# Kernel tuning notes

Hardware: AMD Instinct MI355X
Metric: run time of the kernel (lower is better)

Reference implementation:

```python
import jax, jax.numpy as jnp
import numpy as np

L, B, S, D, H, FF = 6, 32, 512, 512, 8, 2048
DK = D // H
EPS = 1e-5
GELU_C = 0.7978845608028654  # sqrt(2/pi)
INV_SQRT_DK = 1.0 / float(np.sqrt(DK))


def gelu(x):
    return 0.5 * x * (1.0 + jnp.tanh(GELU_C * (x + 0.044715 * x ** 3)))


def layernorm(x, gamma, beta):
    m = jnp.mean(x, axis=-1, keepdims=True)
    v = jnp.mean(jnp.square(x - m), axis=-1, keepdims=True)
    return gamma * (x - m) / jnp.sqrt(v + EPS) + beta


def attention(x, WQ, WK, WV, WO):
    # NOTE: the original splits columns as (d_key, n_heads) on input,
    # and merges as (n_heads * d_key) on output -- replicated faithfully.
    q = (x @ WQ).reshape(B, S, DK, H).transpose(0, 3, 1, 2)  # (B,H,S,DK)
    k = (x @ WK).reshape(B, S, DK, H).transpose(0, 3, 2, 1)  # (B,H,DK,S)
    v = (x @ WV).reshape(B, S, DK, H).transpose(0, 3, 1, 2)  # (B,H,S,DK)
    score = jax.nn.softmax(jnp.matmul(q, k) * INV_SQRT_DK, axis=-1)  # (B,H,S,S)
    o = jnp.matmul(score, v).transpose(0, 2, 1, 3).reshape(B, S, H * DK)
    return o @ WO


def setup_inputs() -> dict:
    key = jax.random.key(0)
    ks = jax.random.split(key, 8)
    sc = 0.02
    return {
        "x": jax.random.normal(ks[0], (B, S, D), jnp.float32),
        "WQ": jax.random.normal(ks[1], (L, D, D), jnp.float32) * sc,
        "WK": jax.random.normal(ks[2], (L, D, D), jnp.float32) * sc,
        "WV": jax.random.normal(ks[3], (L, D, D), jnp.float32) * sc,
        "WO": jax.random.normal(ks[4], (L, D, D), jnp.float32) * sc,
        "K1": jax.random.normal(ks[5], (L, D, FF), jnp.float32) * sc,
        "B1": jnp.zeros((L, FF), jnp.float32),
        "K2": jax.random.normal(ks[6], (L, FF, D), jnp.float32) * sc,
        "B2": jnp.zeros((L, D), jnp.float32),
        "G1": jnp.ones((L, D), jnp.float32),
        "BE1": jnp.zeros((L, D), jnp.float32),
        "G2": jnp.ones((L, D), jnp.float32),
        "BE2": jnp.zeros((L, D), jnp.float32),
    }


def reference(x, WQ, WK, WV, WO, K1, B1, K2, B2, G1, BE1, G2, BE2):
    def step(h, p):
        wq, wk, wv, wo, k1, b1, k2, b2, g1, be1, g2, be2 = p
        h = layernorm(h + attention(h, wq, wk, wv, wo), g1, be1)
        f = gelu(h @ k1 + b1) @ k2 + b2
        h = layernorm(h + f, g2, be2)
        return h, None

    out, _ = jax.lax.scan(step, x, (WQ, WK, WV, WO, K1, B1, K2, B2, G1, BE1, G2, BE2))
    return out
```

## Files before the change

### kernel.cpp

```cpp
#include <hip/hip_runtime.h>
#include <hip/hip_bf16.h>
#include <stdint.h>

#define LB 6
#define BB 32
#define SS 512
#define DD 512
#define HH 8
#define FF_ 2048
#define MM (BB*SS)

typedef unsigned short u16;
typedef __attribute__((ext_vector_type(8))) short bf16x8;
typedef __attribute__((ext_vector_type(4))) float f32x4;

#define MFMA16(a,b,c) __builtin_amdgcn_mfma_f32_16x16x32_bf16((a),(b),(c),0,0,0)
#define GLD16(g, l) __builtin_amdgcn_global_load_lds( \
    (const __attribute__((address_space(1))) unsigned int*)(g), \
    (__attribute__((address_space(3))) unsigned int*)(l), 16, 0, 0)

__device__ __forceinline__ u16 f2b(float f){
  unsigned int u = __float_as_uint(f);
  u = u + 0x7FFFu + ((u >> 16) & 1u);
  return (u16)(u >> 16);
}

__device__ __forceinline__ float gelu_f(float x){
  float u = 0.7978845608028654f * (x + 0.044715f * x * x * x);
  return 0.5f * x * (1.0f + tanhf(u));
}

__global__ __launch_bounds__(256) void k_prep(const float* __restrict__ x,
                                              float* __restrict__ h,
                                              u16* __restrict__ hb){
  int i = blockIdx.x * 256 + threadIdx.x;
  float4 v = ((const float4*)x)[i];
  ((float4*)h)[i] = v;
  uint2 p;
  p.x = (unsigned)f2b(v.x) | ((unsigned)f2b(v.y) << 16);
  p.y = (unsigned)f2b(v.z) | ((unsigned)f2b(v.w) << 16);
  ((uint2*)hb)[i] = p;
}

__global__ __launch_bounds__(256) void k_wt(const float* __restrict__ in,
                                            u16* __restrict__ out, int K, int N){
  size_t ms = (size_t)K * N;
  in  += ms * blockIdx.z;
  out += ms * blockIdx.z;
  int n0 = blockIdx.x * 64, k0 = blockIdx.y * 64;
  __shared__ float tile[64][65];
  int t = threadIdx.x;
  int c = t & 63, rb = t >> 6;
  #pragma unroll
  for (int p = 0; p < 16; p++){
    int k = p * 4 + rb;
    tile[k][c] = in[(size_t)(k0 + k) * N + (n0 + c)];
  }
  __syncthreads();
  #pragma unroll
  for (int p = 0; p < 16; p++){
    int n = p * 4 + rb;
    out[(size_t)(n0 + n) * K + (k0 + c)] = f2b(tile[c][n]);
  }
}

template<int EPI, bool PERM>
__device__ __forceinline__ void gemm_body(const u16* __restrict__ A, const u16* __restrict__ Bt,
    const float* __restrict__ bias, float* __restrict__ outF, u16* __restrict__ outH,
    int N, int K)
{
  __shared__ u16 sA[128*32];
  __shared__ u16 sB[128*32];
  const int t = threadIdx.x;
  const int w = t >> 6, lane = t & 63, lr = lane & 15, lh = lane >> 4;
  const int bm = blockIdx.x * 128, bn = blockIdx.y * 128;
  const int wr = (w >> 1) * 64, wc = (w & 1) * 64;

  f32x4 acc[4][4];
  #pragma unroll
  for (int i = 0; i < 4; i++)
    #pragma unroll
    for (int j = 0; j < 4; j++) acc[i][j] = (f32x4){0.f,0.f,0.f,0.f};

  const int srow = t >> 2;
  const int scol = (t & 3) * 8;
  int b0 = bn + srow, b1 = bn + srow + 64;
  if (PERM){
    b0 = ((b0 & 63) << 3) | (b0 >> 6);
    b1 = ((b1 & 63) << 3) | (b1 >> 6);
  }
  const u16* gA0 = A  + (size_t)(bm + srow) * K + scol;
  const u16* gA1 = gA0 + (size_t)64 * K;
  const u16* gB0 = Bt + (size_t)b0 * K + scol;
  const u16* gB1 = Bt + (size_t)b1 * K + scol;
  u16* lA = sA + w * 512;
  u16* lB = sB + w * 512;

  for (int k0 = 0; k0 < K; k0 += 32){
    GLD16(gA0 + k0, lA);
    GLD16(gA1 + k0, lA + 2048);
    GLD16(gB0 + k0, lB);
    GLD16(gB1 + k0, lB + 2048);
    __syncthreads();
    bf16x8 af[4], bfr[4];
    #pragma unroll
    for (int i = 0; i < 4; i++) af[i]  = *(const bf16x8*)&sA[(wr + i*16 + lr)*32 + lh*8];
    #pragma unroll
    for (int j = 0; j < 4; j++) bfr[j] = *(const bf16x8*)&sB[(wc + j*16 + lr)*32 + lh*8];
    #pragma unroll
    for (int i = 0; i < 4; i++)
      #pragma unroll
      for (int j = 0; j < 4; j++)
        acc[i][j] = MFMA16(af[i], bfr[j], acc[i][j]);
    __syncthreads();
  }

  #pragma unroll
  for (int i = 0; i < 4; i++){
    int row = bm + wr + i*16 + lh*4;
    #pragma unroll
    for (int j = 0; j < 4; j++){
      int col = bn + wc + j*16 + lr;
      float bv = (EPI >= 2) ? bias[col] : 0.f;
      #pragma unroll
      for (int r = 0; r < 4; r++){
        float v = acc[i][j][r];
        size_t o = (size_t)(row + r) * N + col;
        if (EPI == 0) outH[o] = f2b(v);
        else if (EPI == 1) outF[o] = v;
        else if (EPI == 2) outH[o] = f2b(gelu_f(v + bv));
        else outF[o] = v + bv;
      }
    }
  }
}

template<int EPI>
__global__ __launch_bounds__(256) void k_gemm(const u16* A, const u16* Bt, const float* bias,
                                              float* outF, u16* outH, int N, int K){
  gemm_body<EPI,false>(A, Bt, bias, outF, outH, N, K);
}

__global__ __launch_bounds__(256) void k_qkv(const u16* A, const u16* Bq, const u16* Bk, const u16* Bv,
                                             u16* oq, u16* ok, u16* ov){
  const u16* Bt = (blockIdx.z == 0) ? Bq : (blockIdx.z == 1) ? Bk : Bv;
  u16* out = (blockIdx.z == 0) ? oq : (blockIdx.z == 1) ? ok : ov;
  gemm_body<0,true>(A, Bt, nullptr, nullptr, out, DD, DD);
}

__global__ __launch_bounds__(256) void k_attn(const u16* __restrict__ Q, const u16* __restrict__ Kp,
                                              const u16* __restrict__ V, u16* __restrict__ O){
  const int qt = blockIdx.x, hh = blockIdx.y, b = blockIdx.z;
  __shared__ u16 Qs[64*64];
  __shared__ u16 Ks[64*64];
  __shared__ u16 Vt[64*64];
  __shared__ u16 Ps[64*64];
  const int t = threadIdx.x, w = t >> 6, lane = t & 63, lr = lane & 15, lh = lane >> 4;
  const size_t base = ((size_t)b * SS) * DD + (size_t)hh * 64;

  const int srow = t >> 3;
  const int gcol = (((t & 7) ^ (srow & 7)) << 3);
  {
    const u16* g = Q + base + (size_t)(qt*64 + srow) * DD + gcol;
    GLD16(g,                   Qs + w*512);
    GLD16(g + (size_t)32*DD,   Qs + 2048 + w*512);
  }

  float mreg[4], lreg[4];
  f32x4 ofr[4];
  #pragma unroll
  for (int r = 0; r < 4; r++){ mreg[r] = -1e30f; lreg[r] = 0.f; }
  #pragma unroll
  for (int j = 0; j < 4; j++) ofr[j] = (f32x4){0.f,0.f,0.f,0.f};

  const int qswz = (lr & 7) << 3;

  for (int kt = 0; kt < 8; kt++){
    {
      const u16* g = Kp + base + (size_t)(kt*64 + srow) * DD + gcol;
      GLD16(g,                 Ks + w*512);
      GLD16(g + (size_t)32*DD, Ks + 2048 + w*512);
    }
    {
      const int dk0 = (t & 7) * 8, kv = (t >> 3) * 2;
      const u16* g = V + base + (size_t)(kt*64 + kv) * DD + dk0;
      uint4 r0 = *(const uint4*)g;
      uint4 r1 = *(const uint4*)(g + DD);
      const u16* e0 = (const u16*)&r0;
      const u16* e1 = (const u16*)&r1;
      #pragma unroll
      for (int i = 0; i < 8; i++){
        int dk = dk0 + i;
        int sw = ((((dk >> 3) ^ dk) & 7) << 3);
        *(unsigned int*)&Vt[dk*64 + (kv ^ sw)] =
            (unsigned int)e0[i] | ((unsigned int)e1[i] << 16);
      }
    }
    __syncthreads();

    bf16x8 a0 = *(const bf16x8*)&Qs[(w*16+lr)*64 + ((lh*8) ^ qswz)];
    bf16x8 a1 = *(const bf16x8*)&Qs[(w*16+lr)*64 + ((32 + lh*8) ^ qswz)];
    f32x4 sc[4];
    #pragma unroll
    for (int j = 0; j < 4; j++){
      bf16x8 b0 = *(const bf16x8*)&Ks[(j*16+lr)*64 + ((lh*8) ^ qswz)];
      bf16x8 b1 = *(const bf16x8*)&Ks[(j*16+lr)*64 + ((32 + lh*8) ^ qswz)];
      f32x4 z = (f32x4){0.f,0.f,0.f,0.f};
      z = MFMA16(a0, b0, z);
      z = MFMA16(a1, b1, z);
      sc[j] = z;
    }

    float pr[4][4];
    float esc[4];
    #pragma unroll
    for (int r = 0; r < 4; r++){
      float mx = fmaxf(fmaxf(sc[0][r], sc[1][r]), fmaxf(sc[2][r], sc[3][r]));
      mx = fmaxf(mx, __shfl_xor(mx, 1));
      mx = fmaxf(mx, __shfl_xor(mx, 2));
      mx = fmaxf(mx, __shfl_xor(mx, 4));
      mx = fmaxf(mx, __shfl_xor(mx, 8));
      mx *= 0.125f;
      float m2 = fmaxf(mreg[r], mx);
      float scl = __expf(mreg[r] - m2);
      mreg[r] = m2;
      float s = 0.f;
      #pragma unroll
      for (int j = 0; j < 4; j++){
        float p = __expf(sc[j][r]*0.125f - m2);
        pr[j][r] = p;
        s += p;
      }
      s += __shfl_xor(s, 1);
      s += __shfl_xor(s, 2);
      s += __shfl_xor(s, 4);
      s += __shfl_xor(s, 8);
      lreg[r] = lreg[r]*scl + s;
      esc[r] = scl;
    }

    #pragma unroll
    for (int j = 0; j < 4; j++)
      #pragma unroll
      for (int r = 0; r < 4; r++){
        int prow = w*16 + lh*4 + r;
        int pcol = j*16 + lr;
        Ps[prow*64 + (pcol ^ (((lh*4 + r) & 7) << 3))] = f2b(pr[j][r]);
      }

    #pragma unroll
    for (int j = 0; j < 4; j++)
      #pragma unroll
      for (int r = 0; r < 4; r++) ofr[j][r] *= esc[r];

    bf16x8 pa0 = *(const bf16x8*)&Ps[(w*16+lr)*64 + ((lh*8) ^ qswz)];
    bf16x8 pa1 = *(const bf16x8*)&Ps[(w*16+lr)*64 + ((32 + lh*8) ^ qswz)];
    #pragma unroll
    for (int j = 0; j < 4; j++){
      int dkr = j*16 + lr;
      int sw = ((((dkr >> 3) ^ dkr) & 7) << 3);
      bf16x8 v0 = *(const bf16x8*)&Vt[dkr*64 + ((lh*8) ^ sw)];
      bf16x8 v1 = *(const bf16x8*)&Vt[dkr*64 + ((32 + lh*8) ^ sw)];
      ofr[j] = MFMA16(pa0, v0, ofr[j]);
      ofr[j] = MFMA16(pa1, v1, ofr[j]);
    }
    __syncthreads();
  }

  #pragma unroll
  for (int j = 0; j < 4; j++)
    #pragma unroll
    for (int r = 0; r < 4; r++){
      float v = ofr[j][r] / lreg[r];
      O[base + (size_t)(qt*64 + w*16 + lh*4 + r) * DD + j*16 + lr] = f2b(v);
    }
}

__global__ __launch_bounds__(256) void k_ln(const float* __restrict__ hin, const float* __restrict__ add,
    const float* __restrict__ g, const float* __restrict__ be,
    float* __restrict__ hout, u16* __restrict__ hb){
  const int row = blockIdx.x;
  const int t = threadIdx.x;
  const size_t baseo = (size_t)row * DD;
  float v0 = hin[baseo + t]       + add[baseo + t];
  float v1 = hin[baseo + t + 256] + add[baseo + t + 256];
  float s = v0 + v1, q = v0*v0 + v1*v1;
  #pragma unroll
  for (int m = 32; m >= 1; m >>= 1){ s += __shfl_xor(s, m); q += __shfl_xor(q, m); }
  __shared__ float sh[8];
  const int w = t >> 6;
  if ((t & 63) == 0){ sh[w] = s; sh[4 + w] = q; }
  __syncthreads();
  s = sh[0] + sh[1] + sh[2] + sh[3];
  q = sh[4] + sh[5] + sh[6] + sh[7];
  float mean = s * (1.f/512.f);
  float var  = q * (1.f/512.f) - mean*mean;
  float rstd = rsqrtf(var + 1e-5f);
  float o0 = g[t]     * ((v0 - mean) * rstd) + be[t];
  float o1 = g[t+256] * ((v1 - mean) * rstd) + be[t+256];
  hout[baseo + t]       = o0;
  hout[baseo + t + 256] = o1;
  hb[baseo + t]       = f2b(o0);
  hb[baseo + t + 256] = f2b(o1);
}

extern "C" void kernel_launch(void* const* d_in, const int* in_sizes, int n_in,
                              void* d_out, int out_size, void* d_ws, size_t ws_size,
                              hipStream_t stream){
  const float* x   = (const float*)d_in[0];
  const float* WQ  = (const float*)d_in[1];
  const float* WK  = (const float*)d_in[2];
  const float* WV  = (const float*)d_in[3];
  const float* WO  = (const float*)d_in[4];
  const float* K1  = (const float*)d_in[5];
  const float* B1  = (const float*)d_in[6];
  const float* K2  = (const float*)d_in[7];
  const float* B2  = (const float*)d_in[8];
  const float* G1  = (const float*)d_in[9];
  const float* BE1 = (const float*)d_in[10];
  const float* G2  = (const float*)d_in[11];
  const float* BE2 = (const float*)d_in[12];
  float* hF = (float*)d_out;

  char* wp = (char*)d_ws;
  size_t off = 0;
  auto a16 = [&](size_t elems)->u16*{ u16* p = (u16*)(wp + off); off += elems*sizeof(u16); return p; };
  u16* WQt = a16((size_t)LB*DD*DD);
  u16* WKt = a16((size_t)LB*DD*DD);
  u16* WVt = a16((size_t)LB*DD*DD);
  u16* WOt = a16((size_t)LB*DD*DD);
  u16* K1t = a16((size_t)LB*DD*FF_);
  u16* K2t = a16((size_t)LB*DD*FF_);
  u16* hbf = a16((size_t)MM*DD);
  u16* qbf = a16((size_t)MM*DD);
  u16* kbf = a16((size_t)MM*DD);
  u16* vbf = a16((size_t)MM*DD);
  u16* abf = a16((size_t)MM*DD);
  u16* ff1 = qbf;
  float* tmpF = (float*)(wp + off); off += (size_t)MM*DD*sizeof(float);
  (void)ws_size; (void)in_sizes; (void)n_in; (void)out_size;

  k_prep<<<MM*DD/4/256, 256, 0, stream>>>(x, hF, hbf);
  k_wt<<<dim3(8,8,LB),        256, 0, stream>>>(WQ, WQt, DD, DD);
  k_wt<<<dim3(8,8,LB),        256, 0, stream>>>(WK, WKt, DD, DD);
  k_wt<<<dim3(8,8,LB),        256, 0, stream>>>(WV, WVt, DD, DD);
  k_wt<<<dim3(8,8,LB),        256, 0, stream>>>(WO, WOt, DD, DD);
  k_wt<<<dim3(FF_/64,8,LB),   256, 0, stream>>>(K1, K1t, DD, FF_);
  k_wt<<<dim3(8,FF_/64,LB),   256, 0, stream>>>(K2, K2t, FF_, DD);

  for (int l = 0; l < LB; l++){
    const u16* wq = WQt + (size_t)l*DD*DD;
    const u16* wk = WKt + (size_t)l*DD*DD;
    const u16* wv = WVt + (size_t)l*DD*DD;
    const u16* wo = WOt + (size_t)l*DD*DD;
    const u16* k1 = K1t + (size_t)l*DD*FF_;
    const u16* k2 = K2t + (size_t)l*DD*FF_;

    k_qkv<<<dim3(MM/128, DD/128, 3), 256, 0, stream>>>(hbf, wq, wk, wv, qbf, kbf, vbf);
    k_attn<<<dim3(SS/64, HH, BB), 256, 0, stream>>>(qbf, kbf, vbf, abf);
    k_gemm<1><<<dim3(MM/128, DD/128), 256, 0, stream>>>(abf, wo, nullptr, tmpF, nullptr, DD, DD);
    k_ln<<<MM, 256, 0, stream>>>(hF, tmpF, G1 + l*DD, BE1 + l*DD, hF, hbf);
    k_gemm<2><<<dim3(MM/128, FF_/128), 256, 0, stream>>>(hbf, k1, B1 + (size_t)l*FF_, nullptr, ff1, FF_, DD);
    k_gemm<3><<<dim3(MM/128, DD/128), 256, 0, stream>>>(ff1, k2, B2 + l*DD, tmpF, nullptr, DD, FF_);
    k_ln<<<MM, 256, 0, stream>>>(hF, tmpF, G2 + l*DD, BE2 + l*DD, hF, hbf);
  }
}
```

Baseline: 1.866 ms.

## Double-buffer GEMM LDS tiles, use lane-contiguous layout, and cheaper sigmoid GELU

Splits the shared-memory tiles into two ping-pong buffers so the global-to-LDS loads for the next K-slice are issued while MFMAs run on the current one. This replaces the two barriers per iteration with one per phase. The staging layout now writes each 16-row, 32-K fragment contiguously per wave, so fragment reads become one linear lane*8 access intended to avoid LDS bank conflicts. GELU is rewritten as x*sigmoid(2u) using __expf instead of tanhf, which is mathematically equivalent but slightly less accurate.

```diff
diff --git a/kernel.cpp b/kernel.cpp
--- a/kernel.cpp
+++ b/kernel.cpp
@@ -26,8 +26,8 @@
 }
 
 __device__ __forceinline__ float gelu_f(float x){
-  float u = 0.7978845608028654f * (x + 0.044715f * x * x * x);
-  return 0.5f * x * (1.0f + tanhf(u));
+  float u2 = 1.5957691216057308f * (x + 0.044715f * x * x * x);
+  return x / (1.0f + __expf(-u2));
 }
 
 __global__ __launch_bounds__(256) void k_prep(const float* __restrict__ x,
@@ -69,8 +69,7 @@
     const float* __restrict__ bias, float* __restrict__ outF, u16* __restrict__ outH,
     int N, int K)
 {
-  __shared__ u16 sA[128*32];
-  __shared__ u16 sB[128*32];
+  __shared__ u16 sA0[4096], sB0[4096], sA1[4096], sB1[4096];
   const int t = threadIdx.x;
   const int w = t >> 6, lane = t & 63, lr = lane & 15, lh = lane >> 4;
   const int bm = blockIdx.x * 128, bn = blockIdx.y * 128;
@@ -82,37 +81,51 @@
     #pragma unroll
     for (int j = 0; j < 4; j++) acc[i][j] = (f32x4){0.f,0.f,0.f,0.f};
 
-  const int srow = t >> 2;
-  const int scol = (t & 3) * 8;
-  int b0 = bn + srow, b1 = bn + srow + 64;
+  const int lr_s = t & 15;
+  const int kch  = ((t >> 4) & 3) * 8;
+  const int arow0 = w * 16 + lr_s;
+  int b0 = bn + arow0, b1 = bn + arow0 + 64;
   if (PERM){
     b0 = ((b0 & 63) << 3) | (b0 >> 6);
     b1 = ((b1 & 63) << 3) | (b1 >> 6);
   }
-  const u16* gA0 = A  + (size_t)(bm + srow) * K + scol;
+  const u16* gA0 = A  + (size_t)(bm + arow0) * K + kch;
   const u16* gA1 = gA0 + (size_t)64 * K;
-  const u16* gB0 = Bt + (size_t)b0 * K + scol;
-  const u16* gB1 = Bt + (size_t)b1 * K + scol;
-  u16* lA = sA + w * 512;
-  u16* lB = sB + w * 512;
-
-  for (int k0 = 0; k0 < K; k0 += 32){
-    GLD16(gA0 + k0, lA);
-    GLD16(gA1 + k0, lA + 2048);
-    GLD16(gB0 + k0, lB);
-    GLD16(gB1 + k0, lB + 2048);
-    __syncthreads();
+  const u16* gB0 = Bt + (size_t)b0 * K + kch;
+  const u16* gB1 = Bt + (size_t)b1 * K + kch;
+  const int wofs = w * 512;
+
+  auto stage = [&](u16* dA, u16* dB, int k0){
+    GLD16(gA0 + k0, dA + wofs);
+    GLD16(gA1 + k0, dA + 2048 + wofs);
+    GLD16(gB0 + k0, dB + wofs);
+    GLD16(gB1 + k0, dB + 2048 + wofs);
+  };
+  const int iA = (w >> 1) * 4, iB = (w & 1) * 4;
+  auto phase = [&](const u16* cA, const u16* cB, u16* nA, u16* nB, int knext, bool dostage){
     bf16x8 af[4], bfr[4];
     #pragma unroll
-    for (int i = 0; i < 4; i++) af[i]  = *(const bf16x8*)&sA[(wr + i*16 + lr)*32 + lh*8];
-    #pragma unroll
-    for (int j = 0; j < 4; j++) bfr[j] = *(const bf16x8*)&sB[(wc + j*16 + lr)*32 + lh*8];
+    for (int i = 0; i < 4; i++) af[i]  = *(const bf16x8*)&cA[(iA + i)*512 + lane*8];
+    #pragma unroll
+    for (int j = 0; j < 4; j++) bfr[j] = *(const bf16x8*)&cB[(iB + j)*512 + lane*8];
+    if (dostage) stage(nA, nB, knext);
     #pragma unroll
     for (int i = 0; i < 4; i++)
       #pragma unroll
       for (int j = 0; j < 4; j++)
         acc[i][j] = MFMA16(af[i], bfr[j], acc[i][j]);
+  };
+
+  const int NT = K >> 5;
+  stage(sA0, sB0, 0);
+  __syncthreads();
+  #pragma unroll 1
+  for (int kt = 0; kt < NT; kt += 2){
+    phase(sA0, sB0, sA1, sB1, (kt+1) << 5, true);
     __syncthreads();
+    bool more = (kt + 2 < NT);
+    phase(sA1, sB1, sA0, sB0, (kt+2) << 5, more);
+    if (more) __syncthreads();
   }
 
   #pragma unroll
```

Measured after the change: 2.087 ms. 1.12x slower.
